# Kernel optimization log

Measured on AMD Instinct MI355X. Metric: run time of the kernel, lower is better.

Reference implementation:

```python
import jax, jax.numpy as jnp
import numpy as np

N_ENTITIES = 200_000
N_RELATIONS = 2
EMBED_DIM = 64
N_EDGES = 2_000_000


def setup_inputs() -> dict:
    key = jax.random.key(0)
    k1, k2, k3, k4, k5, k6, k7, k8 = jax.random.split(key, 8)
    edge_index = jax.random.randint(k1, (2, N_EDGES), 0, N_ENTITIES, dtype=jnp.int32)
    edge_type = jax.random.randint(k2, (N_EDGES,), 0, N_RELATIONS, dtype=jnp.int32)
    entity_emb = jax.random.normal(k3, (N_ENTITIES, EMBED_DIM), dtype=jnp.float32)
    relation_emb = jax.random.normal(k4, (N_RELATIONS, EMBED_DIM), dtype=jnp.float32)
    att_w = jax.random.normal(k5, (2 * EMBED_DIM, 1), dtype=jnp.float32) * 0.08
    att_b = jax.random.normal(k6, (1,), dtype=jnp.float32) * 0.08
    W_w = jax.random.normal(k7, (EMBED_DIM, EMBED_DIM), dtype=jnp.float32) * 0.12
    W_b = jax.random.normal(k8, (EMBED_DIM,), dtype=jnp.float32) * 0.12
    return {
        "edge_index": edge_index,
        "edge_type": edge_type,
        "entity_emb": entity_emb,
        "relation_emb": relation_emb,
        "att_w": att_w,
        "att_b": att_b,
        "W_w": W_w,
        "W_b": W_b,
    }


def reference(edge_index, edge_type, entity_emb, relation_emb, att_w, att_b, W_w, W_b):
    # Gather per-edge embeddings: [E, D]
    head = entity_emb[edge_index[0]]
    tail = entity_emb[edge_index[1]]
    rel = relation_emb[edge_type]
    # Attention score per edge: sigmoid(Linear(cat(head, rel)))  -> [E, 1]
    head_rel = jnp.concatenate([head, rel], axis=-1)
    att_scores = jax.nn.sigmoid(head_rel @ att_w + att_b)
    # Weighted messages and scatter-add into head nodes (the Python loop in the
    # original is exactly a segment_sum over head indices).
    neighbor_emb = att_scores * tail  # [E, D]
    aggr_emb = jax.ops.segment_sum(neighbor_emb, edge_index[0], num_segments=N_ENTITIES)
    # Final transform: tanh(W @ aggr + b)
    return jnp.tanh(aggr_emb @ W_w.T + W_b)
```

## Files before the change

### kernel.cpp

```cpp
#include <hip/hip_runtime.h>
#include <hip/hip_bf16.h>


#define DIM 64
#define TMASK 0x3FFFF
#define RBIT (1 << 18)
#define BSH 8
#define NBK_MAX 800
#define CHUNK 6144
#define SCAN_ITEMS 4

__global__ __launch_bounds__(256) void kgat_hdot(
    const float* __restrict__ emb, const float* __restrict__ rel,
    const float* __restrict__ att_w, const float* __restrict__ att_b,
    float* __restrict__ hdot, float* __restrict__ rb,
    int n_ent, int n_rel) {
  int gid = blockIdx.x * 256 + threadIdx.x;
  int n = gid >> 4;
  int q = threadIdx.x & 15;
  if (n >= n_ent + n_rel) return;
  float4 v, w;
  if (n < n_ent) {
    v = ((const float4*)emb)[n * 16 + q];
    w = ((const float4*)att_w)[q];
  } else {
    v = ((const float4*)rel)[(n - n_ent) * 16 + q];
    w = ((const float4*)att_w)[16 + q];
  }
  float p = v.x * w.x + v.y * w.y + v.z * w.z + v.w * w.w;
  p += __shfl_xor(p, 1);
  p += __shfl_xor(p, 2);
  p += __shfl_xor(p, 4);
  p += __shfl_xor(p, 8);
  if (q == 0) {
    if (n < n_ent) hdot[n] = p;
    else rb[n - n_ent] = p + att_b[0];
  }
}

__global__ __launch_bounds__(256) void kgat_bhist(
    const int* __restrict__ ei, int* __restrict__ bcnt, int E, int nbk) {
  __shared__ int hist[NBK_MAX];
  for (int i = threadIdx.x; i < NBK_MAX; i += 256) hist[i] = 0;
  __syncthreads();
  int base = blockIdx.x * CHUNK;
  for (int i = threadIdx.x; i < CHUNK; i += 256) {
    int e = base + i;
    if (e < E) atomicAdd(&hist[ei[e] >> BSH], 1);
  }
  __syncthreads();
  for (int b = threadIdx.x; b < nbk; b += 256) {
    int c = hist[b];
    if (c) atomicAdd(&bcnt[b << 4], c);
  }
}

__global__ __launch_bounds__(256) void kgat_bscan(
    const int* __restrict__ bcnt, int* __restrict__ boff,
    int* __restrict__ gcur, int nbk) {
  __shared__ int sblk[256];
  int v[SCAN_ITEMS];
  int s = 0;
#pragma unroll
  for (int k = 0; k < SCAN_ITEMS; ++k) {
    int idx = threadIdx.x * SCAN_ITEMS + k;
    v[k] = (idx < nbk) ? bcnt[idx << 4] : 0;
    s += v[k];
  }
  sblk[threadIdx.x] = s;
  __syncthreads();
  for (int d = 1; d < 256; d <<= 1) {
    int t = (threadIdx.x >= (unsigned)d) ? sblk[threadIdx.x - d] : 0;
    __syncthreads();
    sblk[threadIdx.x] += t;
    __syncthreads();
  }
  int excl = sblk[threadIdx.x] - s;
#pragma unroll
  for (int k = 0; k < SCAN_ITEMS; ++k) {
    int idx = threadIdx.x * SCAN_ITEMS + k;
    if (idx < nbk) {
      boff[idx] = excl;
      gcur[idx << 4] = excl;
    }
    excl += v[k];
  }
  if (threadIdx.x == 255) boff[nbk] = excl;
}

__global__ __launch_bounds__(256) void kgat_scatter1(
    const int* __restrict__ ei, const int* __restrict__ et,
    int* __restrict__ gcur, int* __restrict__ stage, int E, int nbk) {
  __shared__ int hist[NBK_MAX];
  __shared__ int lstart[NBK_MAX];
  __shared__ int lcur[NBK_MAX];
  __shared__ int sblk[256];
  __shared__ int vals[CHUNK];
  __shared__ unsigned short bid[CHUNK];
  int base = blockIdx.x * CHUNK;
  for (int i = threadIdx.x; i < NBK_MAX; i += 256) hist[i] = 0;
  __syncthreads();
  for (int i = threadIdx.x; i < CHUNK; i += 256) {
    int e = base + i;
    if (e < E) atomicAdd(&hist[ei[e] >> BSH], 1);
  }
  __syncthreads();
  int v[SCAN_ITEMS];
  int s = 0;
#pragma unroll
  for (int k = 0; k < SCAN_ITEMS; ++k) {
    int idx = threadIdx.x * SCAN_ITEMS + k;
    v[k] = (idx < nbk) ? hist[idx] : 0;
    s += v[k];
  }
  sblk[threadIdx.x] = s;
  __syncthreads();
  for (int d = 1; d < 256; d <<= 1) {
    int t = (threadIdx.x >= (unsigned)d) ? sblk[threadIdx.x - d] : 0;
    __syncthreads();
    sblk[threadIdx.x] += t;
    __syncthreads();
  }
  int excl = sblk[threadIdx.x] - s;
#pragma unroll
  for (int k = 0; k < SCAN_ITEMS; ++k) {
    int idx = threadIdx.x * SCAN_ITEMS + k;
    if (idx < nbk) {
      lstart[idx] = excl;
      lcur[idx] = excl;
    }
    excl += v[k];
  }
  __syncthreads();
  for (int b = threadIdx.x; b < nbk; b += 256) {
    int c = hist[b];
    hist[b] = c ? atomicAdd(&gcur[b << 4], c) : 0;
  }
  __syncthreads();
  for (int i = threadIdx.x; i < CHUNK; i += 256) {
    int e = base + i;
    if (e < E) {
      int h = ei[e];
      int t = ei[E + e];
      int r = et[e];
      int b = h >> BSH;
      int pos = atomicAdd(&lcur[b], 1);
      vals[pos] = t | (r << 18) | ((h & 255) << 19);
      bid[pos] = (unsigned short)b;
    }
  }
  __syncthreads();
  int cc = E - base;
  if (cc > CHUNK) cc = CHUNK;
  for (int p = threadIdx.x; p < cc; p += 256) {
    int b = bid[p];
    stage[hist[b] + (p - lstart[b])] = vals[p];
  }
}

__global__ __launch_bounds__(256) void kgat_scatter2(
    const int* __restrict__ stage, const int* __restrict__ boff,
    int* __restrict__ off, int* __restrict__ payload) {
  __shared__ int hist[256];
  __shared__ int sc[256];
  __shared__ int lcur[256];
  int b = blockIdx.x;
  int tid = threadIdx.x;
  int s0 = boff[b], s1 = boff[b + 1];
  hist[tid] = 0;
  __syncthreads();
  for (int p = s0 + tid; p < s1; p += 256)
    atomicAdd(&hist[(stage[p] >> 19) & 255], 1);
  __syncthreads();
  int c = hist[tid];
  sc[tid] = c;
  __syncthreads();
  for (int d = 1; d < 256; d <<= 1) {
    int t = (tid >= d) ? sc[tid - d] : 0;
    __syncthreads();
    sc[tid] += t;
    __syncthreads();
  }
  int basep = s0 + sc[tid] - c;
  off[(b << 8) + tid] = basep;
  lcur[tid] = basep;
  __syncthreads();
  for (int p = s0 + tid; p < s1; p += 256) {
    int vv = stage[p];
    int pos = atomicAdd(&lcur[(vv >> 19) & 255], 1);
    payload[pos] = vv;
  }
}

__global__ __launch_bounds__(256) void kgat_aggr_fused(
    const int* __restrict__ off, const int* __restrict__ payload,
    const float* __restrict__ emb, const float* __restrict__ hdot,
    const float* __restrict__ rb, const float* __restrict__ Ww,
    const float* __restrict__ Wb, float* __restrict__ out, int n) {
  __shared__ float Ws[64][68];
  for (int idx = threadIdx.x; idx < 64 * 64; idx += 256) {
    int j = idx >> 6, i = idx & 63;
    Ws[i][j] = Ww[idx];
  }
  __syncthreads();
  int q = threadIdx.x & 15;
  int grp = threadIdx.x >> 4;
  int lanebase = (threadIdx.x & 63) & ~15;
  int stride = gridDim.x * 16;
  float r0 = rb[0], r1 = rb[1];
  float4 bb = ((const float4*)Wb)[q];
  const float4* emb4 = (const float4*)emb;
  for (int h = blockIdx.x * 16 + grp; h < n; h += stride) {
    int p = off[h];
    int p1 = off[h + 1];
    float hd = hdot[h];
    float sc0 = 1.0f / (1.0f + __expf(-(hd + r0)));
    float sc1 = 1.0f / (1.0f + __expf(-(hd + r1)));
    float4 acc = make_float4(0.f, 0.f, 0.f, 0.f);
    for (; p + 4 <= p1; p += 4) {
      int v0 = payload[p + 0];
      int v1 = payload[p + 1];
      int v2 = payload[p + 2];
      int v3 = payload[p + 3];
      float4 t0 = emb4[(v0 & TMASK) * 16 + q];
      float4 t1 = emb4[(v1 & TMASK) * 16 + q];
      float4 t2 = emb4[(v2 & TMASK) * 16 + q];
      float4 t3 = emb4[(v3 & TMASK) * 16 + q];
      float s0 = (v0 & RBIT) ? sc1 : sc0;
      float s1 = (v1 & RBIT) ? sc1 : sc0;
      float s2 = (v2 & RBIT) ? sc1 : sc0;
      float s3 = (v3 & RBIT) ? sc1 : sc0;
      acc.x = fmaf(s0, t0.x, acc.x); acc.y = fmaf(s0, t0.y, acc.y);
      acc.z = fmaf(s0, t0.z, acc.z); acc.w = fmaf(s0, t0.w, acc.w);
      acc.x = fmaf(s1, t1.x, acc.x); acc.y = fmaf(s1, t1.y, acc.y);
      acc.z = fmaf(s1, t1.z, acc.z); acc.w = fmaf(s1, t1.w, acc.w);
      acc.x = fmaf(s2, t2.x, acc.x); acc.y = fmaf(s2, t2.y, acc.y);
      acc.z = fmaf(s2, t2.z, acc.z); acc.w = fmaf(s2, t2.w, acc.w);
      acc.x = fmaf(s3, t3.x, acc.x); acc.y = fmaf(s3, t3.y, acc.y);
      acc.z = fmaf(s3, t3.z, acc.z); acc.w = fmaf(s3, t3.w, acc.w);
    }
    for (; p < p1; ++p) {
      int v0 = payload[p];
      float s0 = (v0 & RBIT) ? sc1 : sc0;
      float4 t0 = emb4[(v0 & TMASK) * 16 + q];
      acc.x = fmaf(s0, t0.x, acc.x); acc.y = fmaf(s0, t0.y, acc.y);
      acc.z = fmaf(s0, t0.z, acc.z); acc.w = fmaf(s0, t0.w, acc.w);
    }
    float4 o = bb;
#pragma unroll 4
    for (int j = 0; j < 16; ++j) {
      float a0 = __shfl(acc.x, lanebase + j);
      float a1 = __shfl(acc.y, lanebase + j);
      float a2 = __shfl(acc.z, lanebase + j);
      float a3 = __shfl(acc.w, lanebase + j);
      float4 w0 = *(const float4*)&Ws[4 * j + 0][4 * q];
      float4 w1 = *(const float4*)&Ws[4 * j + 1][4 * q];
      float4 w2 = *(const float4*)&Ws[4 * j + 2][4 * q];
      float4 w3 = *(const float4*)&Ws[4 * j + 3][4 * q];
      o.x = fmaf(a0, w0.x, o.x); o.y = fmaf(a0, w0.y, o.y);
      o.z = fmaf(a0, w0.z, o.z); o.w = fmaf(a0, w0.w, o.w);
      o.x = fmaf(a1, w1.x, o.x); o.y = fmaf(a1, w1.y, o.y);
      o.z = fmaf(a1, w1.z, o.z); o.w = fmaf(a1, w1.w, o.w);
      o.x = fmaf(a2, w2.x, o.x); o.y = fmaf(a2, w2.y, o.y);
      o.z = fmaf(a2, w2.z, o.z); o.w = fmaf(a2, w2.w, o.w);
      o.x = fmaf(a3, w3.x, o.x); o.y = fmaf(a3, w3.y, o.y);
      o.z = fmaf(a3, w3.z, o.z); o.w = fmaf(a3, w3.w, o.w);
    }
    o.x = tanhf(o.x); o.y = tanhf(o.y); o.z = tanhf(o.z); o.w = tanhf(o.w);
    ((float4*)out)[h * 16 + q] = o;
  }
}

extern "C" void kernel_launch(void* const* d_in, const int* in_sizes, int n_in,
                              void* d_out, int out_size, void* d_ws, size_t ws_size,
                              hipStream_t stream) {
  const int* edge_index = (const int*)d_in[0];
  const int* edge_type  = (const int*)d_in[1];
  const float* entity_emb   = (const float*)d_in[2];
  const float* relation_emb = (const float*)d_in[3];
  const float* att_w = (const float*)d_in[4];
  const float* att_b = (const float*)d_in[5];
  const float* W_w   = (const float*)d_in[6];
  const float* W_b   = (const float*)d_in[7];
  float* out = (float*)d_out;

  const int E     = in_sizes[0] / 2;
  const int N_ENT = in_sizes[2] / DIM;
  const int N_REL = in_sizes[3] / DIM;
  const int NBK   = (N_ENT + 255) >> BSH;

  int* w32 = (int*)d_ws;
  float* hdot = (float*)w32;
  float* rb   = (float*)(w32 + N_ENT);
  int*   bcnt = w32 + N_ENT + 8;
  int*   boff = bcnt + NBK * 16;
  int*   gcur = boff + NBK + 1;
  int*   off  = gcur + NBK * 16;
  int*   stage   = off + NBK * 256 + 1;
  int*   payload = stage + E;

  hipMemsetAsync(bcnt, 0, (size_t)NBK * 16 * sizeof(int), stream);

  {
    int blocks = ((N_ENT + N_REL) * 16 + 255) / 256;
    kgat_hdot<<<blocks, 256, 0, stream>>>(entity_emb, relation_emb, att_w, att_b,
                                          hdot, rb, N_ENT, N_REL);
  }
  int eblocks = (E + CHUNK - 1) / CHUNK;
  kgat_bhist<<<eblocks, 256, 0, stream>>>(edge_index, bcnt, E, NBK);
  kgat_bscan<<<1, 256, 0, stream>>>(bcnt, boff, gcur, NBK);
  kgat_scatter1<<<eblocks, 256, 0, stream>>>(edge_index, edge_type, gcur, stage, E, NBK);
  kgat_scatter2<<<NBK, 256, 0, stream>>>(stage, boff, off, payload);
  kgat_aggr_fused<<<2048, 256, 0, stream>>>(off, payload, entity_emb, hdot, rb,
                                            W_w, W_b, out, N_ENT);
}
```

Before: 186.9 us.

## Gather tail embeddings from an fp16 copy and merge the hdot and histogram kernels

The hdot pass now also writes an fp16 copy of the entity embeddings into workspace. When the workspace is large enough, the aggregation kernel gathers tail rows from that copy, halving the bytes moved by the random gathers. The hdot and bucket-histogram kernels are merged into one launch, and the gather loop is unrolled from 4 to 8 edges. The cost is an extra 25.6 MB write, fp16 rounding error in the aggregated messages, and more registers per thread.

```diff
diff --git a/kernel.cpp b/kernel.cpp
--- a/kernel.cpp
+++ b/kernel.cpp
@@ -1,5 +1,6 @@
 #include <hip/hip_runtime.h>
 #include <hip/hip_bf16.h>
+#include <hip/hip_fp16.h>
 
 
 #define DIM 64
@@ -10,48 +11,65 @@
 #define CHUNK 6144
 #define SCAN_ITEMS 4
 
-__global__ __launch_bounds__(256) void kgat_hdot(
+static __device__ __forceinline__ float4 h4tof4(uint2 u) {
+  __half2 a = *reinterpret_cast<__half2*>(&u.x);
+  __half2 b = *reinterpret_cast<__half2*>(&u.y);
+  float2 fa = __half22float2(a);
+  float2 fb = __half22float2(b);
+  return make_float4(fa.x, fa.y, fb.x, fb.y);
+}
+
+__global__ __launch_bounds__(256) void kgat_front(
     const float* __restrict__ emb, const float* __restrict__ rel,
     const float* __restrict__ att_w, const float* __restrict__ att_b,
+    const int* __restrict__ ei,
     float* __restrict__ hdot, float* __restrict__ rb,
-    int n_ent, int n_rel) {
-  int gid = blockIdx.x * 256 + threadIdx.x;
-  int n = gid >> 4;
-  int q = threadIdx.x & 15;
-  if (n >= n_ent + n_rel) return;
-  float4 v, w;
-  if (n < n_ent) {
-    v = ((const float4*)emb)[n * 16 + q];
-    w = ((const float4*)att_w)[q];
+    __half* __restrict__ emb16, int* __restrict__ bcnt,
+    int n_ent, int n_rel, int E, int nbk, int hblocks) {
+  __shared__ int hist[NBK_MAX];
+  if ((int)blockIdx.x < hblocks) {
+    int gid = blockIdx.x * 256 + threadIdx.x;
+    int n = gid >> 4;
+    int q = threadIdx.x & 15;
+    if (n >= n_ent + n_rel) return;
+    float4 v, w;
+    if (n < n_ent) {
+      v = ((const float4*)emb)[n * 16 + q];
+      w = ((const float4*)att_w)[q];
+      if (emb16) {
+        __half2 h0 = __floats2half2_rn(v.x, v.y);
+        __half2 h1 = __floats2half2_rn(v.z, v.w);
+        uint2 o;
+        o.x = *reinterpret_cast<unsigned int*>(&h0);
+        o.y = *reinterpret_cast<unsigned int*>(&h1);
+        ((uint2*)emb16)[n * 16 + q] = o;
+      }
+    } else {
+      v = ((const float4*)rel)[(n - n_ent) * 16 + q];
+      w = ((const float4*)att_w)[16 + q];
+    }
+    float p = v.x * w.x + v.y * w.y + v.z * w.z + v.w * w.w;
+    p += __shfl_xor(p, 1);
+    p += __shfl_xor(p, 2);
+    p += __shfl_xor(p, 4);
+    p += __shfl_xor(p, 8);
+    if (q == 0) {
+      if (n < n_ent) hdot[n] = p;
+      else rb[n - n_ent] = p + att_b[0];
+    }
   } else {
-    v = ((const float4*)rel)[(n - n_ent) * 16 + q];
-    w = ((const float4*)att_w)[16 + q];
-  }
-  float p = v.x * w.x + v.y * w.y + v.z * w.z + v.w * w.w;
-  p += __shfl_xor(p, 1);
-  p += __shfl_xor(p, 2);
-  p += __shfl_xor(p, 4);
-  p += __shfl_xor(p, 8);
-  if (q == 0) {
-    if (n < n_ent) hdot[n] = p;
-    else rb[n - n_ent] = p + att_b[0];
-  }
-}
-
-__global__ __launch_bounds__(256) void kgat_bhist(
-    const int* __restrict__ ei, int* __restrict__ bcnt, int E, int nbk) {
-  __shared__ int hist[NBK_MAX];
-  for (int i = threadIdx.x; i < NBK_MAX; i += 256) hist[i] = 0;
-  __syncthreads();
-  int base = blockIdx.x * CHUNK;
-  for (int i = threadIdx.x; i < CHUNK; i += 256) {
-    int e = base + i;
-    if (e < E) atomicAdd(&hist[ei[e] >> BSH], 1);
-  }
-  __syncthreads();
-  for (int b = threadIdx.x; b < nbk; b += 256) {
-    int c = hist[b];
-    if (c) atomicAdd(&bcnt[b << 4], c);
+    for (int i = threadIdx.x; i < NBK_MAX; i += 256) hist[i] = 0;
+    __syncthreads();
+    int base = ((int)blockIdx.x - hblocks) * CHUNK;
+    for (int i = threadIdx.x; i < CHUNK; i += 256) {
+      int e = base + i;
+      if (e < E) atomicAdd(&hist[ei[e] >> BSH], 1);
+    }
+    __syncthreads();
+    for (int b = threadIdx.x; b < nbk; b += 256) {
+      int c = hist[b];
+      if (c) atomicAdd(&bcnt[b << 4], c);
+    }
   }
 }
 
@@ -192,11 +210,13 @@
   }
 }
 
+template <int USE_FP16>
 __global__ __launch_bounds__(256) void kgat_aggr_fused(
     const int* __restrict__ off, const int* __restrict__ payload,
-    const float* __restrict__ emb, const float* __restrict__ hdot,
-    const float* __restrict__ rb, const float* __restrict__ Ww,
-    const float* __restrict__ Wb, float* __restrict__ out, int n) {
+    const float* __restrict__ emb, const __half* __restrict__ emb16,
+    const float* __restrict__ hdot, const float* __restrict__ rb,
+    const float* __restrict__ Ww, const float* __restrict__ Wb,
+    float* __restrict__ out, int n) {
   __shared__ float Ws[64][68];
   for (int idx = threadIdx.x; idx < 64 * 64; idx += 256) {
     int j = idx >> 6, i = idx & 63;
@@ -210,6 +230,7 @@
   float r0 = rb[0], r1 = rb[1];
   float4 bb = ((const float4*)Wb)[q];
   const float4* emb4 = (const float4*)emb;
+  const uint2* e16 = (const uint2*)emb16;
   for (int h = blockIdx.x * 16 + grp; h < n; h += stride) {
     int p = off[h];
     int p1 = off[h + 1];
@@ -217,19 +238,41 @@
     float sc0 = 1.0f / (1.0f + __expf(-(hd + r0)));
     float sc1 = 1.0f / (1.0f + __expf(-(hd + r1)));
     float4 acc = make_float4(0.f, 0.f, 0.f, 0.f);
-    for (; p + 4 <= p1; p += 4) {
-      int v0 = payload[p + 0];
-      int v1 = payload[p + 1];
-      int v2 = payload[p + 2];
-      int v3 = payload[p + 3];
-      float4 t0 = emb4[(v0 & TMASK) * 16 + q];
-      float4 t1 = emb4[(v1 & TMASK) * 16 + q];
-      float4 t2 = emb4[(v2 & TMASK) * 16 + q];
-      float4 t3 = emb4[(v3 & TMASK) * 16 + q];
+    for (; p + 8 <= p1; p += 8) {
+      int v0 = payload[p + 0], v1 = payload[p + 1];
+      int v2 = payload[p + 2], v3 = payload[p + 3];
+      int v4 = payload[p + 4], v5 = payload[p + 5];
+      int v6 = payload[p + 6], v7 = payload[p + 7];
+      float4 t0, t1, t2, t3, t4, t5, t6, t7;
+      if constexpr (USE_FP16) {
+        uint2 u0 = e16[(v0 & TMASK) * 16 + q];
+        uint2 u1 = e16[(v1 & TMASK) * 16 + q];
+        uint2 u2 = e16[(v2 & TMASK) * 16 + q];
+        uint2 u3 = e16[(v3 & TMASK) * 16 + q];
+        uint2 u4 = e16[(v4 & TMASK) * 16 + q];
+        uint2 u5 = e16[(v5 & TMASK) * 16 + q];
+        uint2 u6 = e16[(v6 & TMASK) * 16 + q];
+        uint2 u7 = e16[(v7 & TMASK) * 16 + q];
+        t0 = h4tof4(u0); t1 = h4tof4(u1); t2 = h4tof4(u2); t3 = h4tof4(u3);
+        t4 = h4tof4(u4); t5 = h4tof4(u5); t6 = h4tof4(u6); t7 = h4tof4(u7);
+      } else {
+        t0 = emb4[(v0 & TMASK) * 16 + q];
+        t1 = emb4[(v1 & TMASK) * 16 + q];
+        t2 = emb4[(v2 & TMASK) * 16 + q];
+        t3 = emb4[(v3 & TMASK) * 16 + q];
+        t4 = emb4[(v4 & TMASK) * 16 + q];
+        t5 = emb4[(v5 & TMASK) * 16 + q];
+        t6 = emb4[(v6 & TMASK) * 16 + q];
+        t7 = emb4[(v7 & TMASK) * 16 + q];
+      }
       float s0 = (v0 & RBIT) ? sc1 : sc0;
       float s1 = (v1 & RBIT) ? sc1 : sc0;
       float s2 = (v2 & RBIT) ? sc1 : sc0;
       float s3 = (v3 & RBIT) ? sc1 : sc0;
+      float s4 = (v4 & RBIT) ? sc1 : sc0;
+      float s5 = (v5 & RBIT) ? sc1 : sc0;
+      float s6 = (v6 & RBIT) ? sc1 : sc0;
+      float s7 = (v7 & RBIT) ? sc1 : sc0;
       acc.x = fmaf(s0, t0.x, acc.x); acc.y = fmaf(s0, t0.y, acc.y);
       acc.z = fmaf(s0, t0.z, acc.z); acc.w = fmaf(s0, t0.w, acc.w);
       acc.x = fmaf(s1, t1.x, acc.x); acc.y = fmaf(s1, t1.y, acc.y);
@@ -238,11 +281,25 @@
       acc.z = fmaf(s2, t2.z, acc.z); acc.w = fmaf(s2, t2.w, acc.w);
       acc.x = fmaf(s3, t3.x, acc.x); acc.y = fmaf(s3, t3.y, acc.y);
       acc.z = fmaf(s3, t3.z, acc.z); acc.w = fmaf(s3, t3.w, acc.w);
+      acc.x = fmaf(s4, t4.x, acc.x); acc.y = fmaf(s4, t4.y, acc.y);
+      acc.z = fmaf(s4, t4.z, acc.z); acc.w = fmaf(s4, t4.w, acc.w);
+      acc.x = fmaf(s5, t5.x, acc.x); acc.y = fmaf(s5, t5.y, acc.y);
+      acc.z = fmaf(s5, t5.z, acc.z); acc.w = fmaf(s5, t5.w, acc.w);
+      acc.x = fmaf(s6, t6.x, acc.x); acc.y = fmaf(s6, t6.y, acc.y);
+      acc.z = fmaf(s6, t6.z, acc.z); acc.w = fmaf(s6, t6.w, acc.w);
+      acc.x = fmaf(s7, t7.x, acc.x); acc.y = fmaf(s7, t7.y, acc.y);
+      acc.z = fmaf(s7, t7.z, acc.z); acc.w = fmaf(s7, t7.w, acc.w);
     }
     for (; p < p1; ++p) {
       int v0 = payload[p];
       float s0 = (v0 & RBIT) ? sc1 : sc0;
-      float4 t0 = emb4[(v0 & TMASK) * 16 + q];
+      float4 t0;
+      if constexpr (USE_FP16) {
+        uint2 u0 = e16[(v0 & TMASK) * 16 + q];
+        t0 = h4tof4(u0);
+      } else {
+        t0 = emb4[(v0 & TMASK) * 16 + q];
+      }
       acc.x = fmaf(s0, t0.x, acc.x); acc.y = fmaf(s0, t0.y, acc.y);
       acc.z = fmaf(s0, t0.z, acc.z); acc.w = fmaf(s0, t0.w, acc.w);
     }
@@ -298,19 +355,28 @@
   int*   off  = gcur + NBK * 16;
   int*   stage   = off + NBK * 256 + 1;
   int*   payload = stage + E;
+  __half* emb16  = (__half*)(payload + E);
+
+  size_t need = ((size_t)N_ENT + 8 + (size_t)NBK * 33 + 2 + (size_t)NBK * 256 +
+                 2 * (size_t)E + (size_t)N_ENT * 32) * 4;
+  const int use16 = (ws_size >= need) ? 1 : 0;
+  if (!use16) emb16 = nullptr;
 
   hipMemsetAsync(bcnt, 0, (size_t)NBK * 16 * sizeof(int), stream);
 
-  {
-    int blocks = ((N_ENT + N_REL) * 16 + 255) / 256;
-    kgat_hdot<<<blocks, 256, 0, stream>>>(entity_emb, relation_emb, att_w, att_b,
-                                          hdot, rb, N_ENT, N_REL);
-  }
+  int hblocks = ((N_ENT + N_REL) * 16 + 255) / 256;
   int eblocks = (E + CHUNK - 1) / CHUNK;
-  kgat_bhist<<<eblocks, 256, 0, stream>>>(edge_index, bcnt, E, NBK);
+  kgat_front<<<hblocks + eblocks, 256, 0, stream>>>(
+      entity_emb, relation_emb, att_w, att_b, edge_index,
+      hdot, rb, emb16, bcnt, N_ENT, N_REL, E, NBK, hblocks);
   kgat_bscan<<<1, 256, 0, stream>>>(bcnt, boff, gcur, NBK);
   kgat_scatter1<<<eblocks, 256, 0, stream>>>(edge_index, edge_type, gcur, stage, E, NBK);
   kgat_scatter2<<<NBK, 256, 0, stream>>>(stage, boff, off, payload);
-  kgat_aggr_fused<<<2048, 256, 0, stream>>>(off, payload, entity_emb, hdot, rb,
-                                            W_w, W_b, out, N_ENT);
-}
+  if (use16) {
+    kgat_aggr_fused<1><<<2048, 256, 0, stream>>>(off, payload, entity_emb, emb16,
+                                                 hdot, rb, W_w, W_b, out, N_ENT);
+  } else {
+    kgat_aggr_fused<0><<<2048, 256, 0, stream>>>(off, payload, entity_emb, nullptr,
+                                                 hdot, rb, W_w, W_b, out, N_ENT);
+  }
+}
```

After: 210.0 us. 1.12x slower.
